# Kernel optimization log

Hardware: AMD Instinct MI355X
Metric: run time of the kernel (lower is better)

Reference implementation:

```python
import jax, jax.numpy as jnp
import numpy as np

ALPHA = 3.0


def _conv3x3(x, W, b):
    # x: [N, C, H, W]; W: [O, I, 3, 3]; SAME padding, stride 1 (matches Conv2d(dim, dim, 3, 1, 1))
    y = jax.lax.conv_general_dilated(
        x, W, window_strides=(1, 1), padding='SAME',
        dimension_numbers=('NCHW', 'OIHW', 'NCHW'))
    return y + b[None, :, None, None]


def setup_inputs() -> dict:
    key = jax.random.key(0)
    k = jax.random.split(key, 5)
    b, m, z, x, y = 2, 5, 64, 128, 256
    fan_in = z * 3 * 3
    bound = 1.0 / np.sqrt(fan_in)
    pts = jax.random.normal(k[0], (b, m, z, x, y), dtype=jnp.float32)
    W1 = jax.random.uniform(k[1], (z, z, 3, 3), jnp.float32, -bound, bound)
    b1 = jax.random.uniform(k[2], (z,), jnp.float32, -bound, bound)
    W2 = jax.random.uniform(k[3], (z, z, 3, 3), jnp.float32, -bound, bound)
    b2 = jax.random.uniform(k[4], (z,), jnp.float32, -bound, bound)
    return {"pts": pts, "W1": W1, "b1": b1, "W2": W2, "b2": b2}


def reference(pts, W1, b1, W2, b2):
    b, m, z, x, y = pts.shape
    flat = pts.reshape(b * m, z, x, y)
    n1 = jnp.tanh(ALPHA * _conv3x3(flat, W1, b1)).reshape(b, m, z, x, y)
    n2 = jnp.tanh(ALPHA * _conv3x3(flat, W2, b2)).reshape(b, m, z, x, y)
    # s[b,m,n,x,y] = sum_l n1[b,m,l,x,y] * n2[b,n,l,x,y]; second einsum is s with m,n swapped
    s = jnp.einsum('bmlxy,bnlxy->bmnxy', n1, n2)
    a = s - jnp.swapaxes(s, 1, 2)
    adj = jax.nn.sigmoid(ALPHA * a)
    adj = adj + jnp.eye(m, dtype=adj.dtype)[None, :, :, None, None]
    adj = adj / jnp.sum(adj, axis=2, keepdims=True)
    return adj
```

## Files before the change

kernel.cpp:

```cpp
#include <hip/hip_runtime.h>
#include <hip/hip_bf16.h>

typedef _Float16 f16x8 __attribute__((ext_vector_type(8)));
typedef float f32x4 __attribute__((ext_vector_type(4)));

constexpr int B_ = 2, M_ = 5, C_ = 64, H_ = 128, W_ = 256;
constexpr int HW_ = H_ * W_;
constexpr int PLANE_ = C_ * HW_;
constexpr int NIMG_ = B_ * M_;
constexpr int PH_ = H_ + 2, PW_ = W_ + 2;

constexpr size_t OFF_XIN = 256;
constexpr size_t SZ_XIN  = (size_t)NIMG_ * PH_ * PW_ * 64 * 2;
constexpr size_t OFF_WL1 = OFF_XIN + SZ_XIN;
constexpr size_t SZ_WL   = (size_t)9 * 64 * 64 * 2;
constexpr size_t OFF_WL2 = OFF_WL1 + SZ_WL;
constexpr size_t OFF_N1  = OFF_WL2 + SZ_WL;
constexpr size_t SZ_N    = (size_t)NIMG_ * HW_ * 64 * 2;
constexpr size_t OFF_N2  = OFF_N1 + SZ_N;

__global__ void sniff_kernel(const unsigned short* __restrict__ pts,
                             int* __restrict__ flag) {
  int lane = threadIdx.x;
  unsigned short v = pts[2 * lane];
  int e = (v >> 7) & 0xFF;
  unsigned long long mask = __ballot(e >= 100 && e <= 140);
  if (lane == 0) flag[0] = (__popcll(mask) >= 48) ? 1 : 0;
}

__global__ void border_zero(_Float16* __restrict__ x) {
  int idx = blockIdx.x * 256 + threadIdx.x;
  if (idx >= NIMG_ * 772) return;
  int img = idx / 772, r = idx - img * 772;
  int ph, pw;
  if (r < 258)      { ph = 0;            pw = r; }
  else if (r < 516) { ph = PH_ - 1;      pw = r - 258; }
  else if (r < 644) { ph = r - 516 + 1;  pw = 0; }
  else              { ph = r - 644 + 1;  pw = PW_ - 1; }
  f16x8 z = {};
  _Float16* p = x + ((size_t)(img * PH_ + ph) * PW_ + pw) * 64;
#pragma unroll
  for (int c8 = 0; c8 < 8; ++c8) *(f16x8*)(p + c8 * 8) = z;
}

__global__ __launch_bounds__(256) void prep_kernel(const void* __restrict__ in,
                                                   _Float16* __restrict__ xin,
                                                   const int* __restrict__ flag) {
  __shared__ float sT[64 * 65];
  const int t = threadIdx.x;
  const int wt = blockIdx.x, h = blockIdx.y, img = blockIdx.z;
  const bool isb = flag[0] != 0;
  const size_t ibase = (size_t)img * PLANE_ + (size_t)h * W_ + wt * 64;
#pragma unroll
  for (int k = 0; k < 16; ++k) {
    int idx = k * 256 + t;
    int ic = idx >> 6, w = idx & 63;
    size_t g = ibase + (size_t)ic * HW_ + w;
    float v = isb ? __bfloat162float(((const __hip_bfloat16*)in)[g])
                  : ((const float*)in)[g];
    sT[ic * 65 + w] = v;
  }
  __syncthreads();
#pragma unroll
  for (int k = 0; k < 2; ++k) {
    int idx = k * 256 + t;
    int w = idx >> 3, c8 = idx & 7;
    f16x8 vv;
#pragma unroll
    for (int j = 0; j < 8; ++j) vv[j] = (_Float16)sT[(c8 * 8 + j) * 65 + w];
    int pw = wt * 64 + w + 1;
    size_t rowbase = ((size_t)(img * PH_ + (h + 1)) * PW_ + pw) * 128;
    int off = (c8 * 16) ^ ((pw & 7) << 4);
    *(f16x8*)((char*)xin + rowbase + off) = vv;
  }
}

__global__ void wprep_kernel(const void* __restrict__ W1, const void* __restrict__ W2,
                             _Float16* __restrict__ wl1, _Float16* __restrict__ wl2,
                             const int* __restrict__ flag) {
  int idx = blockIdx.x * 256 + threadIdx.x;
  const bool isb = flag[0] != 0;
  const void* Wsrc = blockIdx.y ? W2 : W1;
  _Float16* dst = blockIdx.y ? wl2 : wl1;
  int tap = idx >> 12;
  int oc = (idx >> 6) & 63;
  int ic = idx & 63;
  size_t s = (size_t)(oc * 64 + ic) * 9 + tap;
  float v = isb ? __bfloat162float(((const __hip_bfloat16*)Wsrc)[s])
                : ((const float*)Wsrc)[s];
  dst[(tap * 4096 + oc * 64 + ic) ^ ((oc & 7) << 3)] = (_Float16)v;
}

__global__ __launch_bounds__(512, 2)
void conv_fused(const _Float16* __restrict__ xin,
                const _Float16* __restrict__ wl1, const _Float16* __restrict__ wl2,
                const void* __restrict__ bias1, const void* __restrict__ bias2,
                const int* __restrict__ flag,
                _Float16* __restrict__ n1, _Float16* __restrict__ n2) {
  __shared__ _Float16 sIn[10 * 66 * 64];
  __shared__ _Float16 sW[2 * 9 * 32 * 64];

  const int t = threadIdx.x;
  const int och = blockIdx.x & 1;
  const int pid = blockIdx.x >> 1;

  const int l = t & 63, wv = t >> 6;
  const int lr = l & 15, hi = l >> 4;
  const bool isb = flag[0] != 0;

#pragma unroll
  for (int c = 0; c < 2; ++c) {
    const f16x8* src = (const f16x8*)((const char*)(c ? wl2 : wl1) + och * 4096);
    f16x8* dst = (f16x8*)sW + c * 2304;
    for (int i = t; i < 2304; i += 512) {
      int tap = i >> 8, e = i & 255;
      dst[i] = src[tap * 512 + e];
    }
  }

  float bv1[2], bv2[2];
#pragma unroll
  for (int ob = 0; ob < 2; ++ob) {
    int oc = och * 32 + ob * 16 + lr;
    bv1[ob] = isb ? __bfloat162float(((const __hip_bfloat16*)bias1)[oc])
                  : ((const float*)bias1)[oc];
    bv2[ob] = isb ? __bfloat162float(((const __hip_bfloat16*)bias2)[oc])
                  : ((const float*)bias2)[oc];
  }

  int c2a[3][2], c2b[2];
#pragma unroll
  for (int dx = 0; dx < 3; ++dx) {
    int key = (((l & 7) + dx) & 7) << 4;
#pragma unroll
    for (int kw = 0; kw < 2; ++kw) c2a[dx][kw] = (hi * 16 + kw * 64) ^ key;
  }
#pragma unroll
  for (int kw = 0; kw < 2; ++kw) c2b[kw] = (hi * 16 + kw * 64) ^ ((l & 7) << 4);

  f16x8 rg[11];
  auto issue = [&](int tt) {
    int img = tt >> 6, hy = (tt >> 2) & 15, wx = tt & 3;
    const f16x8* base = (const f16x8*)(xin + ((size_t)(img * PH_ + hy * 8) * PW_ + wx * 64) * 64);
#pragma unroll
    for (int u = 0; u < 11; ++u) {
      int i = u * 512 + t;
      if (u < 10 || i < 5280) {
        int r = i / 528, cc = i - r * 528;
        rg[u] = base[(size_t)r * (PW_ * 8) + cc];
      }
    }
  };

  issue(pid);

  const char* sInB = (const char*)sIn;
  const char* sWB = (const char*)sW;

#pragma unroll 1
  for (int j = 0; j < 5; ++j) {
    const int tt = pid + 128 * j;

#pragma unroll
    for (int u = 0; u < 11; ++u) {
      int i = u * 512 + t;
      if (u < 10 || i < 5280) ((f16x8*)sIn)[i] = rg[u];
    }
    __syncthreads();

    if (j < 4) issue(pid + 128 * (j + 1));

    f32x4 acc1[4][2], acc2[4][2];
#pragma unroll
    for (int pa = 0; pa < 4; ++pa)
#pragma unroll
      for (int ob = 0; ob < 2; ++ob) {
        acc1[pa][ob] = (f32x4){0.f, 0.f, 0.f, 0.f};
        acc2[pa][ob] = (f32x4){0.f, 0.f, 0.f, 0.f};
      }

#pragma unroll
    for (int ky = 0; ky < 3; ++ky) {
#pragma unroll
      for (int kx = 0; kx < 3; ++kx) {
        const int tap = ky * 3 + kx;
#pragma unroll
        for (int kw = 0; kw < 2; ++kw) {
          f16x8 a[4], b1[2], b2[2];
#pragma unroll
          for (int pa = 0; pa < 4; ++pa)
            a[pa] = *(const f16x8*)(sInB + ((wv + ky) * 8448 + (pa * 16 + lr + kx) * 128 + c2a[kx][kw]));
#pragma unroll
          for (int ob = 0; ob < 2; ++ob) {
            b1[ob] = *(const f16x8*)(sWB + (tap * 4096 + (ob * 16 + lr) * 128 + c2b[kw]));
            b2[ob] = *(const f16x8*)(sWB + (36864 + tap * 4096 + (ob * 16 + lr) * 128 + c2b[kw]));
          }
#pragma unroll
          for (int pa = 0; pa < 4; ++pa)
#pragma unroll
            for (int ob = 0; ob < 2; ++ob) {
              acc1[pa][ob] = __builtin_amdgcn_mfma_f32_16x16x32_f16(a[pa], b1[ob], acc1[pa][ob], 0, 0, 0);
              acc2[pa][ob] = __builtin_amdgcn_mfma_f32_16x16x32_f16(a[pa], b2[ob], acc2[pa][ob], 0, 0, 0);
            }
        }
      }
    }

    {
      int img = tt >> 6, hy = (tt >> 2) & 15, wx = tt & 3;
      size_t rowbase = ((size_t)(img * H_ + hy * 8 + wv) * W_ + wx * 64) * 64 + och * 32 + lr;
#pragma unroll
      for (int pa = 0; pa < 4; ++pa)
#pragma unroll
        for (int ob = 0; ob < 2; ++ob)
#pragma unroll
          for (int r = 0; r < 4; ++r) {
            int px = pa * 16 + hi * 4 + r;
            size_t o = rowbase + (size_t)px * 64 + ob * 16;
            float u1 = acc1[pa][ob][r] + bv1[ob];
            u1 = fminf(fmaxf(u1, -8.f), 8.f);
            float e1 = __builtin_exp2f(u1 * -8.656170245f);
            n1[o] = (_Float16)((1.f - e1) * __builtin_amdgcn_rcpf(1.f + e1));
            float u2 = acc2[pa][ob][r] + bv2[ob];
            u2 = fminf(fmaxf(u2, -8.f), 8.f);
            float e2 = __builtin_exp2f(u2 * -8.656170245f);
            n2[o] = (_Float16)((1.f - e2) * __builtin_amdgcn_rcpf(1.f + e2));
          }
    }
    __syncthreads();
  }
}

__global__ __launch_bounds__(256)
void pairwise_kernel(const _Float16* __restrict__ n1, const _Float16* __restrict__ n2,
                     void* __restrict__ out, const int* __restrict__ flag) {
  int tid = blockIdx.x * 256 + threadIdx.x;
  int gp = tid >> 3;
  int j = tid & 7;
  int b = gp >> 15, px = gp & (HW_ - 1);
  const _Float16* p1 = n1 + ((size_t)(b * M_) * HW_ + px) * 64 + j * 8;
  const _Float16* p2 = n2 + ((size_t)(b * M_) * HW_ + px) * 64 + j * 8;

  f16x8 A[M_], Bv[M_];
#pragma unroll
  for (int m = 0; m < M_; ++m) {
    A[m]  = *(const f16x8*)(p1 + (size_t)m * PLANE_);
    Bv[m] = *(const f16x8*)(p2 + (size_t)m * PLANE_);
  }

  float s[M_][M_];
#pragma unroll
  for (int m = 0; m < M_; ++m)
#pragma unroll
    for (int n = 0; n < M_; ++n) s[m][n] = 0.f;

#pragma unroll
  for (int jj = 0; jj < 8; ++jj)
#pragma unroll
    for (int m = 0; m < M_; ++m)
#pragma unroll
      for (int n = 0; n < M_; ++n)
        s[m][n] += (float)A[m][jj] * (float)Bv[n][jj];

#pragma unroll
  for (int m = 0; m < M_; ++m)
#pragma unroll
    for (int n = 0; n < M_; ++n) {
      s[m][n] += __shfl_xor(s[m][n], 1);
      s[m][n] += __shfl_xor(s[m][n], 2);
      s[m][n] += __shfl_xor(s[m][n], 4);
    }

  float adj[M_][M_], rs[M_];
#pragma unroll
  for (int m = 0; m < M_; ++m) {
    float r = 0.f;
#pragma unroll
    for (int n = 0; n < M_; ++n) {
      float a = s[m][n] - s[n][m];
      float e = __builtin_exp2f(a * -4.328085123f);
      float v = __builtin_amdgcn_rcpf(1.f + e);
      if (m == n) v += 1.f;
      adj[m][n] = v;
      r += v;
    }
    rs[m] = r;
  }

  const bool isb = flag[0] != 0;
  for (int k = j; k < 25; k += 8) {
    int m = k / 5, n = k - m * 5;
    float v = adj[m][n] * __builtin_amdgcn_rcpf(rs[m]);
    size_t o = ((size_t)((b * M_ + m) * M_ + n)) * HW_ + px;
    if (isb) ((__hip_bfloat16*)out)[o] = __float2bfloat16(v);
    else     ((float*)out)[o] = v;
  }
}

extern "C" void kernel_launch(void* const* d_in, const int* in_sizes, int n_in,
                              void* d_out, int out_size, void* d_ws, size_t ws_size,
                              hipStream_t stream) {
  const void* pts = d_in[0];
  const void* W1  = d_in[1];
  const void* b1  = d_in[2];
  const void* W2  = d_in[3];
  const void* b2  = d_in[4];

  char* ws = (char*)d_ws;
  int* flag = (int*)ws;
  _Float16* xin = (_Float16*)(ws + OFF_XIN);
  _Float16* wl1 = (_Float16*)(ws + OFF_WL1);
  _Float16* wl2 = (_Float16*)(ws + OFF_WL2);
  _Float16* n1  = (_Float16*)(ws + OFF_N1);
  _Float16* n2  = (_Float16*)(ws + OFF_N2);

  sniff_kernel<<<dim3(1), dim3(64), 0, stream>>>((const unsigned short*)pts, flag);
  border_zero<<<dim3((NIMG_ * 772 + 255) / 256), dim3(256), 0, stream>>>(xin);
  prep_kernel<<<dim3(4, H_, NIMG_), dim3(256), 0, stream>>>(pts, xin, flag);
  wprep_kernel<<<dim3(144, 2), dim3(256), 0, stream>>>(W1, W2, wl1, wl2, flag);
  conv_fused<<<dim3(256), dim3(512), 0, stream>>>(xin, wl1, wl2, b1, b2, flag, n1, n2);
  pairwise_kernel<<<dim3(B_ * HW_ * 8 / 256), dim3(256), 0, stream>>>(n1, n2, d_out, flag);
}
```

Baseline: 134.7 us.

## Merge border zeroing into weight prep and streamline conv loop barriers

Folds the padding-border zeroing into the weight-prep kernel, which removes one kernel launch. In the conv loop, accumulators are initialised with the bias, and the tanh epilogue is rewritten as 1-2/(1+e^{2x}) without clamping. The __syncthreads pair is replaced by an explicit lgkmcnt wait plus s_barrier placed before the epilogue, and s_setprio is raised around the MFMA block. Removing the clamp risks inf/NaN handling differences for large inputs; rcp(inf)=0 should still yield 1, and the barrier reordering needs care with LDS reuse.

```diff
diff --git a/kernel.cpp b/kernel.cpp
--- a/kernel.cpp
+++ b/kernel.cpp
@@ -28,21 +28,6 @@
   if (lane == 0) flag[0] = (__popcll(mask) >= 48) ? 1 : 0;
 }
 
-__global__ void border_zero(_Float16* __restrict__ x) {
-  int idx = blockIdx.x * 256 + threadIdx.x;
-  if (idx >= NIMG_ * 772) return;
-  int img = idx / 772, r = idx - img * 772;
-  int ph, pw;
-  if (r < 258)      { ph = 0;            pw = r; }
-  else if (r < 516) { ph = PH_ - 1;      pw = r - 258; }
-  else if (r < 644) { ph = r - 516 + 1;  pw = 0; }
-  else              { ph = r - 644 + 1;  pw = PW_ - 1; }
-  f16x8 z = {};
-  _Float16* p = x + ((size_t)(img * PH_ + ph) * PW_ + pw) * 64;
-#pragma unroll
-  for (int c8 = 0; c8 < 8; ++c8) *(f16x8*)(p + c8 * 8) = z;
-}
-
 __global__ __launch_bounds__(256) void prep_kernel(const void* __restrict__ in,
                                                    _Float16* __restrict__ xin,
                                                    const int* __restrict__ flag) {
@@ -77,8 +62,26 @@
 
 __global__ void wprep_kernel(const void* __restrict__ W1, const void* __restrict__ W2,
                              _Float16* __restrict__ wl1, _Float16* __restrict__ wl2,
+                             _Float16* __restrict__ xin,
                              const int* __restrict__ flag) {
-  int idx = blockIdx.x * 256 + threadIdx.x;
+  const int t = threadIdx.x;
+  if (blockIdx.x >= 144) {
+    if (blockIdx.y != 0) return;
+    int idx = (blockIdx.x - 144) * 256 + t;
+    if (idx >= NIMG_ * 772) return;
+    int img = idx / 772, r = idx - img * 772;
+    int ph, pw;
+    if (r < 258)      { ph = 0;            pw = r; }
+    else if (r < 516) { ph = PH_ - 1;      pw = r - 258; }
+    else if (r < 644) { ph = r - 516 + 1;  pw = 0; }
+    else              { ph = r - 644 + 1;  pw = PW_ - 1; }
+    f16x8 z = {};
+    _Float16* p = xin + ((size_t)(img * PH_ + ph) * PW_ + pw) * 64;
+#pragma unroll
+    for (int c8 = 0; c8 < 8; ++c8) *(f16x8*)(p + c8 * 8) = z;
+    return;
+  }
+  int idx = blockIdx.x * 256 + t;
   const bool isb = flag[0] != 0;
   const void* Wsrc = blockIdx.y ? W2 : W1;
   _Float16* dst = blockIdx.y ? wl2 : wl1;
@@ -157,6 +160,8 @@
   const char* sInB = (const char*)sIn;
   const char* sWB = (const char*)sW;
 
+  __syncthreads();
+
 #pragma unroll 1
   for (int j = 0; j < 5; ++j) {
     const int tt = pid + 128 * j;
@@ -166,7 +171,8 @@
       int i = u * 512 + t;
       if (u < 10 || i < 5280) ((f16x8*)sIn)[i] = rg[u];
     }
-    __syncthreads();
+    asm volatile("s_waitcnt lgkmcnt(0)" ::: "memory");
+    __builtin_amdgcn_s_barrier();
 
     if (j < 4) issue(pid + 128 * (j + 1));
 
@@ -175,10 +181,11 @@
     for (int pa = 0; pa < 4; ++pa)
 #pragma unroll
       for (int ob = 0; ob < 2; ++ob) {
-        acc1[pa][ob] = (f32x4){0.f, 0.f, 0.f, 0.f};
-        acc2[pa][ob] = (f32x4){0.f, 0.f, 0.f, 0.f};
+        acc1[pa][ob] = (f32x4){bv1[ob], bv1[ob], bv1[ob], bv1[ob]};
+        acc2[pa][ob] = (f32x4){bv2[ob], bv2[ob], bv2[ob], bv2[ob]};
       }
 
+    __builtin_amdgcn_s_setprio(1);
 #pragma unroll
     for (int ky = 0; ky < 3; ++ky) {
 #pragma unroll
@@ -186,29 +193,32 @@
         const int tap = ky * 3 + kx;
 #pragma unroll
         for (int kw = 0; kw < 2; ++kw) {
-          f16x8 a[4], b1[2], b2[2];
+          f16x8 a[4], b1a, b1b, b2a, b2b;
 #pragma unroll
           for (int pa = 0; pa < 4; ++pa)
             a[pa] = *(const f16x8*)(sInB + ((wv + ky) * 8448 + (pa * 16 + lr + kx) * 128 + c2a[kx][kw]));
-#pragma unroll
-          for (int ob = 0; ob < 2; ++ob) {
-            b1[ob] = *(const f16x8*)(sWB + (tap * 4096 + (ob * 16 + lr) * 128 + c2b[kw]));
-            b2[ob] = *(const f16x8*)(sWB + (36864 + tap * 4096 + (ob * 16 + lr) * 128 + c2b[kw]));
+          b1a = *(const f16x8*)(sWB + tap * 4096 + lr * 128 + c2b[kw]);
+          b1b = *(const f16x8*)(sWB + tap * 4096 + (16 + lr) * 128 + c2b[kw]);
+          b2a = *(const f16x8*)(sWB + 36864 + tap * 4096 + lr * 128 + c2b[kw]);
+          b2b = *(const f16x8*)(sWB + 36864 + tap * 4096 + (16 + lr) * 128 + c2b[kw]);
+#pragma unroll
+          for (int pa = 0; pa < 4; ++pa) {
+            acc1[pa][0] = __builtin_amdgcn_mfma_f32_16x16x32_f16(a[pa], b1a, acc1[pa][0], 0, 0, 0);
+            acc1[pa][1] = __builtin_amdgcn_mfma_f32_16x16x32_f16(a[pa], b1b, acc1[pa][1], 0, 0, 0);
+            acc2[pa][0] = __builtin_amdgcn_mfma_f32_16x16x32_f16(a[pa], b2a, acc2[pa][0], 0, 0, 0);
+            acc2[pa][1] = __builtin_amdgcn_mfma_f32_16x16x32_f16(a[pa], b2b, acc2[pa][1], 0, 0, 0);
           }
-#pragma unroll
-          for (int pa = 0; pa < 4; ++pa)
-#pragma unroll
-            for (int ob = 0; ob < 2; ++ob) {
-              acc1[pa][ob] = __builtin_amdgcn_mfma_f32_16x16x32_f16(a[pa], b1[ob], acc1[pa][ob], 0, 0, 0);
-              acc2[pa][ob] = __builtin_amdgcn_mfma_f32_16x16x32_f16(a[pa], b2[ob], acc2[pa][ob], 0, 0, 0);
-            }
         }
       }
     }
+    __builtin_amdgcn_s_setprio(0);
+
+    __builtin_amdgcn_s_barrier();
 
     {
       int img = tt >> 6, hy = (tt >> 2) & 15, wx = tt & 3;
-      size_t rowbase = ((size_t)(img * H_ + hy * 8 + wv) * W_ + wx * 64) * 64 + och * 32 + lr;
+      size_t rowbase = ((size_t)(img * H_ + hy * 8 + wv) * W_ + wx * 64) * 64
+                       + och * 32 + lr;
 #pragma unroll
       for (int pa = 0; pa < 4; ++pa)
 #pragma unroll
@@ -217,17 +227,12 @@
           for (int r = 0; r < 4; ++r) {
             int px = pa * 16 + hi * 4 + r;
             size_t o = rowbase + (size_t)px * 64 + ob * 16;
-            float u1 = acc1[pa][ob][r] + bv1[ob];
-            u1 = fminf(fmaxf(u1, -8.f), 8.f);
-            float e1 = __builtin_exp2f(u1 * -8.656170245f);
-            n1[o] = (_Float16)((1.f - e1) * __builtin_amdgcn_rcpf(1.f + e1));
-            float u2 = acc2[pa][ob][r] + bv2[ob];
-            u2 = fminf(fmaxf(u2, -8.f), 8.f);
-            float e2 = __builtin_exp2f(u2 * -8.656170245f);
-            n2[o] = (_Float16)((1.f - e2) * __builtin_amdgcn_rcpf(1.f + e2));
+            float e1 = __builtin_exp2f(acc1[pa][ob][r] * 8.656170245f);
+            n1[o] = (_Float16)fmaf(-2.f, __builtin_amdgcn_rcpf(1.f + e1), 1.f);
+            float e2 = __builtin_exp2f(acc2[pa][ob][r] * 8.656170245f);
+            n2[o] = (_Float16)fmaf(-2.f, __builtin_amdgcn_rcpf(1.f + e2), 1.f);
           }
     }
-    __syncthreads();
   }
 }
 
@@ -315,9 +320,8 @@
   _Float16* n2  = (_Float16*)(ws + OFF_N2);
 
   sniff_kernel<<<dim3(1), dim3(64), 0, stream>>>((const unsigned short*)pts, flag);
-  border_zero<<<dim3((NIMG_ * 772 + 255) / 256), dim3(256), 0, stream>>>(xin);
   prep_kernel<<<dim3(4, H_, NIMG_), dim3(256), 0, stream>>>(pts, xin, flag);
-  wprep_kernel<<<dim3(144, 2), dim3(256), 0, stream>>>(W1, W2, wl1, wl2, flag);
+  wprep_kernel<<<dim3(175, 2), dim3(256), 0, stream>>>(W1, W2, wl1, wl2, xin, flag);
   conv_fused<<<dim3(256), dim3(512), 0, stream>>>(xin, wl1, wl2, b1, b2, flag, n1, n2);
   pairwise_kernel<<<dim3(B_ * HW_ * 8 / 256), dim3(256), 0, stream>>>(n1, n2, d_out, flag);
 }
```

Measured after the change: 130.3 us. 1.03x faster.
